# Performance work log

Hardware: AMD Instinct MI355X
Metric: run time of the kernel (lower is better)

## Reference

```python
import jax, jax.numpy as jnp
import numpy as np

B, T, D = 4, 2048, 2048
NUM_EXPERTS = 64
TOP_K = 2


def setup_inputs() -> dict:
    key = jax.random.key(0)
    k_x, k_n, k_wg, k_wn = jax.random.split(key, 4)
    x = jax.random.normal(k_x, (B, T, D), dtype=jnp.float32)
    noise_eps = jax.random.normal(k_n, (B, T, NUM_EXPERTS), dtype=jnp.float32)
    # nn.Linear(D, E, bias=False): weight [E, D]; store transposed [D, E] for einsum
    scale = 1.0 / np.sqrt(D)
    w_gate = jax.random.uniform(k_wg, (D, NUM_EXPERTS), jnp.float32, -scale, scale)
    w_noise = jax.random.uniform(k_wn, (D, NUM_EXPERTS), jnp.float32, -scale, scale)
    return {"x": x, "noise_eps": noise_eps, "w_gate": w_gate, "w_noise": w_noise}


def reference(x, noise_eps, w_gate, w_noise):
    # gate + noisy logits: softplus(w_noise(x)) * randn_like (noise_eps passed in)
    logits = jnp.einsum("btd,de->bte", x, w_gate)
    noise = jax.nn.softplus(jnp.einsum("btd,de->bte", x, w_noise)) * noise_eps
    logits = logits + noise

    # top-k over experts
    top_k_logits, top_k_indices = jax.lax.top_k(logits, TOP_K)  # [B,T,K]

    # scatter(-inf fill) + softmax == softmax over top-k values scattered into E slots
    one_hot = jax.nn.one_hot(top_k_indices, NUM_EXPERTS, dtype=logits.dtype)  # [B,T,K,E]
    router_probs = jnp.einsum("btk,btke->bte", jax.nn.softmax(top_k_logits, axis=-1), one_hot)

    # per-expert mask: [num_tokens, K, E] -> permute(1,0,2) -> [K, num_tokens, E]
    exp_mask = one_hot.reshape(B * T, TOP_K, NUM_EXPERTS).transpose(1, 0, 2).astype(jnp.int32)
    return router_probs, top_k_indices, exp_mask
```

## Files before the change

### kernel.cpp

```cpp
#include <hip/hip_runtime.h>
#include <math.h>

#define DD     2048
#define EE     64
#define NTOK   8192
#define BM     64
#define KSPLIT 4
#define KQ     512
#define BK     32
#define NCH    (KQ / BK)

#define PROB_OFF 0
#define IDX_OFF  524288
#define MASK_OFF 540672
#define MASK_K_STRIDE (NTOK * EE)

#define XBUF_OFF(b) ((b) * 8192)
#define BBUF_OFF(b) (16384 + (b) * 16384)
#define LDS_BYTES   49152

typedef __bf16 bf16x8 __attribute__((ext_vector_type(8)));
typedef float  f32x16 __attribute__((ext_vector_type(16)));

__device__ __forceinline__ unsigned f2bf_rne(float f) {
  unsigned u = __float_as_uint(f);
  return (u + 0x7fffu + ((u >> 16) & 1u)) >> 16;
}
__device__ __forceinline__ float bf2f(unsigned h) {
  return __uint_as_float(h << 16);
}

__device__ __forceinline__ void gl_lds16(const void* g, void* l) {
  __builtin_amdgcn_global_load_lds(
      (const __attribute__((address_space(1))) unsigned int*)g,
      (__attribute__((address_space(3))) unsigned int*)l,
      16, 0, 0);
}

__global__ __launch_bounds__(256) void prep_w(
    const float* __restrict__ wg, const float* __restrict__ wn,
    unsigned char* __restrict__ wsb)
{
  const int t  = blockIdx.x * 256 + threadIdx.x;
  const int l  = t & 63;
  const int nt = (t >> 6) & 3;
  const int g  = t >> 8;
  const int colg = nt * 32 + (l & 31);
  const int kb   = g * 16 + 8 * (l >> 5);
  const float* wsrc = (colg < EE) ? (wg + colg) : (wn + (colg - EE));

  unsigned hv[8], lv[8];
#pragma unroll
  for (int i = 0; i < 8; ++i) {
    const float v = wsrc[(size_t)(kb + i) * EE];
    const unsigned h = f2bf_rne(v);
    hv[i] = h;
    lv[i] = f2bf_rne(v - bf2f(h));
  }
  uint4 hq, lq;
  hq.x = hv[0] | (hv[1] << 16); hq.y = hv[2] | (hv[3] << 16);
  hq.z = hv[4] | (hv[5] << 16); hq.w = hv[6] | (hv[7] << 16);
  lq.x = lv[0] | (lv[1] << 16); lq.y = lv[2] | (lv[3] << 16);
  lq.z = lv[4] | (lv[5] << 16); lq.w = lv[6] | (lv[7] << 16);

  const size_t base = ((size_t)(g * 4 + nt) * 2) * 1024 + (size_t)l * 16;
  *reinterpret_cast<uint4*>(wsb + base)        = hq;
  *reinterpret_cast<uint4*>(wsb + base + 1024) = lq;
}

union BF8 { bf16x8 v; ushort u[8]; };

__device__ __forceinline__ void cvt_hilo(const float4& a, const float4& b,
                                         bf16x8& hi, bf16x8& lo) {
  const float f[8] = {a.x, a.y, a.z, a.w, b.x, b.y, b.z, b.w};
  BF8 H, L;
#pragma unroll
  for (int i = 0; i < 8; ++i) {
    const unsigned u = __float_as_uint(f[i]);
    H.u[i] = (ushort)(u >> 16);
    L.v[i] = (__bf16)(f[i] - __uint_as_float(u & 0xffff0000u));
  }
  hi = H.v; lo = L.v;
}

__device__ __forceinline__ bf16x8 bc(const uint4& q) {
  return __builtin_bit_cast(bf16x8, q);
}

__global__ __launch_bounds__(512, 4) void router_gemm(
    const float* __restrict__ x,
    const unsigned char* __restrict__ wsb,
    float* __restrict__ part)
{
  __shared__ unsigned char lds[LDS_BYTES];

  const int tid  = threadIdx.x;
  const int wid  = tid >> 6;
  const int lane = tid & 63;
  const int mh   = wid >> 2;
  const int nt   = wid & 3;
  const int tok0 = blockIdx.x * BM;
  const int ks   = blockIdx.y;
  const int kbase = ks * KQ;

  const int xrow  = tid >> 3;
  const int xslot = tid & 7;
  const float* xsrc = x + (size_t)(tok0 + xrow) * DD + kbase
                        + ((xslot ^ (xrow & 7)) << 2);
  const unsigned char* bsrc = wsb + (size_t)(ks * (KQ / 16)) * 8192
                                  + (size_t)tid * 16;

  const int arow = lane & 31;
  const int atl  = lane >> 5;
  const int xswz = arow & 7;

  f32x16 acc = {0.f,0.f,0.f,0.f,0.f,0.f,0.f,0.f,
                0.f,0.f,0.f,0.f,0.f,0.f,0.f,0.f};

  {
    gl_lds16(xsrc, &lds[XBUF_OFF(0) + tid * 16]);
    gl_lds16(bsrc,        &lds[BBUF_OFF(0) + tid * 16]);
    gl_lds16(bsrc + 8192, &lds[BBUF_OFF(0) + 8192 + tid * 16]);
  }
  __syncthreads();

  for (int c = 0; c < NCH; ++c) {
    const int cb = c & 1;

    if (c + 1 < NCH) {
      const int nb = cb ^ 1;
      gl_lds16(xsrc + (c + 1) * BK, &lds[XBUF_OFF(nb) + tid * 16]);
      const unsigned char* bs = bsrc + (size_t)(c + 1) * 16384;
      gl_lds16(bs,        &lds[BBUF_OFF(nb) + tid * 16]);
      gl_lds16(bs + 8192, &lds[BBUF_OFF(nb) + 8192 + tid * 16]);
    }

    const unsigned char* xb = &lds[XBUF_OFF(cb)];
    const unsigned char* bb = &lds[BBUF_OFF(cb)];
#pragma unroll
    for (int s = 0; s < 2; ++s) {
      const int sl0 = (4 * s + 2 * atl) ^ xswz;
      const int sl1 = (4 * s + 2 * atl + 1) ^ xswz;
      const float4 xa = *reinterpret_cast<const float4*>(
          xb + (32 * mh + arow) * 128 + sl0 * 16);
      const float4 xv = *reinterpret_cast<const float4*>(
          xb + (32 * mh + arow) * 128 + sl1 * 16);
      const unsigned char* q = bb + s * 8192 + nt * 2048 + lane * 16;
      const uint4 bh = *reinterpret_cast<const uint4*>(q);
      const uint4 bl = *reinterpret_cast<const uint4*>(q + 1024);

      bf16x8 ahi, alo;
      cvt_hilo(xa, xv, ahi, alo);
      acc = __builtin_amdgcn_mfma_f32_32x32x16_bf16(ahi, bc(bh), acc, 0, 0, 0);
      acc = __builtin_amdgcn_mfma_f32_32x32x16_bf16(ahi, bc(bl), acc, 0, 0, 0);
      acc = __builtin_amdgcn_mfma_f32_32x32x16_bf16(alo, bc(bh), acc, 0, 0, 0);
    }
    __syncthreads();
  }

  float* Lp = reinterpret_cast<float*>(lds);
  const int ccol = nt * 32 + (lane & 31);
#pragma unroll
  for (int q = 0; q < 16; ++q) {
    const int r = 32 * mh + (q & 3) + 8 * (q >> 2) + 4 * atl;
    Lp[r * 128 + ccol] = acc[q];
  }
  __syncthreads();
#pragma unroll
  for (int rr = 0; rr < 8; ++rr) {
    const int r = 8 * wid + rr;
    const float2 v = *reinterpret_cast<const float2*>(&Lp[r * 128 + 2 * lane]);
    *reinterpret_cast<float2*>(
        part + ((size_t)(tok0 + r) * KSPLIT + ks) * 128 + 2 * lane) = v;
  }
}

__global__ __launch_bounds__(256) void router_epilogue(
    const float* __restrict__ part,
    const float* __restrict__ noise_eps,
    float* __restrict__ out)
{
  const int t    = blockIdx.x * 4 + (threadIdx.x >> 6);
  const int lane = threadIdx.x & 63;

  const float* p = part + (size_t)t * KSPLIT * 128;
  float g = 0.0f, nraw = 0.0f;
#pragma unroll
  for (int s = 0; s < KSPLIT; ++s) {
    g    += p[s * 128 + lane];
    nraw += p[s * 128 + EE + lane];
  }
  const float ep = noise_eps[(size_t)t * EE + lane];

  const float sp = fmaxf(nraw, 0.0f) + log1pf(expf(-fabsf(nraw)));
  const float z  = fmaf(sp, ep, g);

  float v1 = z; int i1 = lane;
#pragma unroll
  for (int off = 32; off >= 1; off >>= 1) {
    const float ov = __shfl_xor(v1, off, 64);
    const int   oi = __shfl_xor(i1, off, 64);
    if (ov > v1 || (ov == v1 && oi < i1)) { v1 = ov; i1 = oi; }
  }
  float v2 = (lane == i1) ? -INFINITY : z; int i2 = lane;
#pragma unroll
  for (int off = 32; off >= 1; off >>= 1) {
    const float ov = __shfl_xor(v2, off, 64);
    const int   oi = __shfl_xor(i2, off, 64);
    if (ov > v2 || (ov == v2 && oi < i2)) { v2 = ov; i2 = oi; }
  }

  const float e2 = expf(v2 - v1);
  const float denom = 1.0f + e2;
  const float p1 = 1.0f / denom;
  const float p2 = e2 / denom;

  out[PROB_OFF + (size_t)t * EE + lane] =
      (lane == i1) ? p1 : ((lane == i2) ? p2 : 0.0f);

  if (lane == 0) {
    out[IDX_OFF + t * 2 + 0] = (float)i1;
    out[IDX_OFF + t * 2 + 1] = (float)i2;
  }

  out[MASK_OFF + 0 * MASK_K_STRIDE + (size_t)t * EE + lane] = (lane == i1) ? 1.0f : 0.0f;
  out[MASK_OFF + 1 * MASK_K_STRIDE + (size_t)t * EE + lane] = (lane == i2) ? 1.0f : 0.0f;
}

extern "C" void kernel_launch(void* const* d_in, const int* in_sizes, int n_in,
                              void* d_out, int out_size, void* d_ws, size_t ws_size,
                              hipStream_t stream) {
  const float* x   = (const float*)d_in[0];
  const float* eps = (const float*)d_in[1];
  const float* wg  = (const float*)d_in[2];
  const float* wn  = (const float*)d_in[3];

  unsigned char* wsb = (unsigned char*)d_ws;
  float* part = (float*)(wsb + (1 << 20));

  prep_w<<<dim3(128), dim3(256), 0, stream>>>(wg, wn, wsb);
  router_gemm<<<dim3(NTOK / BM, KSPLIT), dim3(512), 0, stream>>>(x, wsb, part);
  router_epilogue<<<dim3(NTOK / 4), dim3(256), 0, stream>>>(part, eps,
                                                            (float*)d_out);
}
```

Baseline: 123.5 us.

## Triple-buffer GEMM LDS staging with explicit vmcnt waits

Moves the router GEMM's LDS staging from double to triple buffering. Loads are issued two chunks ahead and guarded by explicit s_waitcnt vmcnt counts plus raw barriers instead of __syncthreads, and the chunk loop is fully unrolled. The aim is to hide global-to-LDS load latency behind MFMA work. In exchange LDS use grows from 48KB to 72KB per block, which can reduce occupancy below the 4 blocks per CU the launch bounds request.

```diff
diff --git a/kernel.cpp b/kernel.cpp
--- a/kernel.cpp
+++ b/kernel.cpp
@@ -16,8 +16,8 @@
 #define MASK_K_STRIDE (NTOK * EE)
 
 #define XBUF_OFF(b) ((b) * 8192)
-#define BBUF_OFF(b) (16384 + (b) * 16384)
-#define LDS_BYTES   49152
+#define BBUF_OFF(b) (24576 + (b) * 16384)
+#define LDS_BYTES   73728
 
 typedef __bf16 bf16x8 __attribute__((ext_vector_type(8)));
 typedef float  f32x16 __attribute__((ext_vector_type(16)));
@@ -117,26 +117,27 @@
   f32x16 acc = {0.f,0.f,0.f,0.f,0.f,0.f,0.f,0.f,
                 0.f,0.f,0.f,0.f,0.f,0.f,0.f,0.f};
 
-  {
-    gl_lds16(xsrc, &lds[XBUF_OFF(0) + tid * 16]);
-    gl_lds16(bsrc,        &lds[BBUF_OFF(0) + tid * 16]);
-    gl_lds16(bsrc + 8192, &lds[BBUF_OFF(0) + 8192 + tid * 16]);
-  }
-  __syncthreads();
-
+  auto STAGE = [&](int cc, int b) {
+    gl_lds16(xsrc + cc * BK, &lds[XBUF_OFF(b) + tid * 16]);
+    const unsigned char* bs = bsrc + (size_t)cc * 16384;
+    gl_lds16(bs,        &lds[BBUF_OFF(b) + tid * 16]);
+    gl_lds16(bs + 8192, &lds[BBUF_OFF(b) + 8192 + tid * 16]);
+  };
+
+  STAGE(0, 0);
+  STAGE(1, 1);
+  STAGE(2, 2);
+
+#pragma unroll
   for (int c = 0; c < NCH; ++c) {
-    const int cb = c & 1;
-
-    if (c + 1 < NCH) {
-      const int nb = cb ^ 1;
-      gl_lds16(xsrc + (c + 1) * BK, &lds[XBUF_OFF(nb) + tid * 16]);
-      const unsigned char* bs = bsrc + (size_t)(c + 1) * 16384;
-      gl_lds16(bs,        &lds[BBUF_OFF(nb) + tid * 16]);
-      gl_lds16(bs + 8192, &lds[BBUF_OFF(nb) + 8192 + tid * 16]);
-    }
-
-    const unsigned char* xb = &lds[XBUF_OFF(cb)];
-    const unsigned char* bb = &lds[BBUF_OFF(cb)];
+    if (c <= NCH - 3)      asm volatile("s_waitcnt vmcnt(6)" ::: "memory");
+    else if (c == NCH - 2) asm volatile("s_waitcnt vmcnt(3)" ::: "memory");
+    else                   asm volatile("s_waitcnt vmcnt(0)" ::: "memory");
+    __builtin_amdgcn_s_barrier();
+    __builtin_amdgcn_sched_barrier(0);
+
+    const unsigned char* xb = &lds[XBUF_OFF(c % 3)];
+    const unsigned char* bb = &lds[BBUF_OFF(c % 3)];
 #pragma unroll
     for (int s = 0; s < 2; ++s) {
       const int sl0 = (4 * s + 2 * atl) ^ xswz;
@@ -155,7 +156,12 @@
       acc = __builtin_amdgcn_mfma_f32_32x32x16_bf16(ahi, bc(bl), acc, 0, 0, 0);
       acc = __builtin_amdgcn_mfma_f32_32x32x16_bf16(alo, bc(bh), acc, 0, 0, 0);
     }
-    __syncthreads();
+
+    asm volatile("s_waitcnt lgkmcnt(0)" ::: "memory");
+    __builtin_amdgcn_s_barrier();
+    __builtin_amdgcn_sched_barrier(0);
+
+    if (c + 3 < NCH) STAGE(c + 3, c % 3);
   }
 
   float* Lp = reinterpret_cast<float*>(lds);
```

Result: no change. 122.5 us (-0.8%).
